# Optimization experiments

Measured on AMD Instinct MI355X. Metric: run time of the kernel, lower is better.

## Reference

```python
import jax, jax.numpy as jnp
import numpy as np

D_MODEL = 1024
D_STATE = 16
DT_RANK = 64  # d_model // 16 ('auto')
DT_MIN = 0.001
DT_MAX = 0.1


def setup_inputs() -> dict:
    key = jax.random.key(0)
    ks = jax.random.split(key, 7)
    B, S = 2, 2048
    return {
        "x": jax.random.normal(ks[0], (B, S, D_MODEL), jnp.float32),
        "w_in": jax.random.normal(ks[1], (D_MODEL, D_MODEL), jnp.float32) / np.sqrt(D_MODEL).astype(np.float32),
        "w_x": jax.random.normal(ks[2], (D_MODEL, DT_RANK + 2 * D_STATE), jnp.float32) / np.sqrt(D_MODEL).astype(np.float32),
        "w_dt": jax.random.normal(ks[3], (DT_RANK, D_MODEL), jnp.float32) / np.sqrt(DT_RANK).astype(np.float32),
        "b_dt": jnp.zeros((D_MODEL,), jnp.float32),
        "A_log": jax.random.normal(ks[5], (D_MODEL, D_STATE), jnp.float32) * 0.5,
        "Dp": jax.random.normal(ks[6], (D_MODEL,), jnp.float32),
    }


def reference(x, w_in, w_x, w_dt, b_dt, A_log, Dp):
    # x: (b, s, d)
    x_in = jnp.einsum('bsd,de->bse', x, w_in)          # in_proj, (b,s,d_inner=d)
    proj = jnp.einsum('bsd,dp->bsp', x_in, w_x)        # x_proj, (b,s,dt_rank+2n)
    dt_low, Bm, Cm = jnp.split(proj, [DT_RANK, DT_RANK + D_STATE], axis=-1)
    # dt_proj + softplus + range scaling -> (b,s,d)
    dt = jax.nn.softplus(jnp.einsum('bsr,rd->bsd', dt_low, w_dt) + b_dt) * (DT_MAX - DT_MIN) + DT_MIN
    A = -jnp.exp(A_log)                                # (d, n), strictly negative

    b, s, d = x.shape
    h0 = jnp.zeros((b, d, D_STATE), x.dtype)

    # time-major streams for scan
    dt_tm = jnp.swapaxes(dt, 0, 1)     # (s,b,d)
    u_tm = jnp.swapaxes(x_in, 0, 1)    # (s,b,d)
    B_tm = jnp.swapaxes(Bm, 0, 1)      # (s,b,n)
    C_tm = jnp.swapaxes(Cm, 0, 1)      # (s,b,n)

    def step(h, inp):
        dtt, ut, bt, ct = inp
        dA = dtt[:, :, None] * A                      # (b,d,n) = dt[b,d]*A[d,n]
        barA = jnp.exp(dA)
        # bar_B = dA; source sums the input term over channel dim d (keepdim)
        inp_term = jnp.einsum('bdn,bn,bd->bn', dA, bt, ut)  # (b,n)
        h = barA * h + inp_term[:, None, :]           # broadcast over d
        y = jnp.einsum('bdn,bn->bd', h, ct) + Dp * ut # (b,d)
        return h, y

    _, ys = jax.lax.scan(step, h0, (dt_tm, u_tm, B_tm, C_tm))  # ys: (s,b,d)
    return jnp.swapaxes(ys, 0, 1)                     # (b,s,d)
```

## Files before the change

kernel.cpp:

```cpp
#include <hip/hip_runtime.h>
#include <hip/hip_bf16.h>

#define D_MODEL 1024
#define D_STATE 16
#define DT_RANK 64
#define SEQ 2048
#define BATCH 2
#define M_TOTAL 4096
#define CHUNKS 64
#define CLEN 32

typedef __bf16 bf16x8 __attribute__((ext_vector_type(8)));
typedef float f32x4 __attribute__((ext_vector_type(4)));

__device__ __forceinline__ unsigned short f2bf(float f) {
    union { float f; unsigned int u; } v; v.f = f;
    unsigned int r = v.u + 0x7FFFu + ((v.u >> 16) & 1u);
    return (unsigned short)(r >> 16);
}
__device__ __forceinline__ float bf2f(unsigned short u) {
    union { unsigned int i; float f; } v; v.i = ((unsigned int)u) << 16; return v.f;
}
__device__ __forceinline__ void gload16(const void* g, void* l) {
    __builtin_amdgcn_global_load_lds(
        (const __attribute__((address_space(1))) unsigned int*)g,
        (__attribute__((address_space(3))) unsigned int*)l, 16, 0, 0);
}

__global__ void __launch_bounds__(256) k_setup(const float* __restrict__ x,
                                               const float* __restrict__ win,
                                               const float* __restrict__ wx,
                                               const float* __restrict__ alog,
                                               unsigned short* __restrict__ xb,
                                               unsigned short* __restrict__ wib,
                                               unsigned short* __restrict__ bt,
                                               unsigned short* __restrict__ wxT,
                                               unsigned short* __restrict__ wxBC,
                                               float* __restrict__ aneg,
                                               unsigned short* __restrict__ anegT) {
    __shared__ float tile[32][33];
    int blk = blockIdx.x;
    int t = threadIdx.x;
    if (blk < 4096) {
        int i = blk * 256 + t;
        float4 v = reinterpret_cast<const float4*>(x)[i];
        ushort4 o;
        o.x = f2bf(v.x); o.y = f2bf(v.y); o.z = f2bf(v.z); o.w = f2bf(v.w);
        reinterpret_cast<ushort4*>(xb)[i] = o;
    } else if (blk < 5120) {
        int i = (blk - 4096) * 256 + t;
        float4 v = reinterpret_cast<const float4*>(win)[i];
        ushort4 o;
        o.x = f2bf(v.x); o.y = f2bf(v.y); o.z = f2bf(v.z); o.w = f2bf(v.w);
        reinterpret_cast<ushort4*>(wib)[i] = o;
    } else if (blk < 6144) {
        int blk2 = blk - 5120;
        int bx = blk2 & 31, by = blk2 >> 5;
        int tx = t & 31, ty = t >> 5;
        int xc = bx * 32 + tx;
#pragma unroll
        for (int j = 0; j < 4; j++)
            tile[ty + 8 * j][tx] = win[(by * 32 + ty + 8 * j) * D_MODEL + xc];
        __syncthreads();
        int x2 = by * 32 + tx;
#pragma unroll
        for (int j = 0; j < 4; j++)
            bt[(bx * 32 + ty + 8 * j) * D_MODEL + x2] = f2bf(tile[tx][ty + 8 * j]);
    } else if (blk < 6400) {
        int idx = (blk - 6144) * 256 + t;
        int e = idx & 1023, p = idx >> 10;
        wxT[p * D_MODEL + e] = f2bf(wx[e * 96 + p]);
    } else if (blk < 6528) {
        int idx = (blk - 6400) * 256 + t;
        int e = idx & 1023, p = idx >> 10;
        wxBC[p * D_MODEL + e] = f2bf(wx[e * 96 + 64 + p]);
    } else {
        int i = (blk - 6528) * 256 + t;
        float v = -expf(alog[i]);
        aneg[i] = v;
        anegT[(i & 15) * D_MODEL + (i >> 4)] = f2bf(v);
    }
}

__global__ void __launch_bounds__(256) k_prepgemm(const unsigned short* __restrict__ wxT,
                                                  const unsigned short* __restrict__ wib,
                                                  float* __restrict__ Cp) {
    __shared__ unsigned short sA[2][64 * 32];
    __shared__ unsigned short sB[2][128 * 32];
    int bid = blockIdx.x;
    int n0 = (bid & 7) * 128;
    int ks = bid >> 3;
    int kbase = ks * 256;
    int t = threadIdx.x;
    int lane = t & 63;
    int w = t >> 6;
    int c = lane & 15, q = lane >> 4;

    const unsigned short* ga = wxT + (t >> 2) * D_MODEL + (t & 3) * 8 + kbase;
    const unsigned short* gb = wib + (n0 + (t >> 2)) * D_MODEL + (t & 3) * 8 + kbase;

    f32x4 acc[4][2] = {};
    {
        char* la = (char*)&sA[0][0] + w * 1024;
        char* lb = (char*)&sB[0][0] + w * 1024;
        gload16(ga, la);
        gload16(gb, lb);
        gload16(gb + 64 * D_MODEL, lb + 4096);
    }
    int cur = 0;
    for (int it = 0; it < 8; it++) {
        __syncthreads();
        if (it + 1 < 8) {
            int kn = (it + 1) * 32;
            char* la = (char*)&sA[cur ^ 1][0] + w * 1024;
            char* lb = (char*)&sB[cur ^ 1][0] + w * 1024;
            gload16(ga + kn, la);
            gload16(gb + kn, lb);
            gload16(gb + 64 * D_MODEL + kn, lb + 4096);
        }
        bf16x8 af[4], bfr[2];
#pragma unroll
        for (int i = 0; i < 4; i++)
            af[i] = *reinterpret_cast<const bf16x8*>(&sA[cur][(i * 16 + c) * 32 + q * 8]);
#pragma unroll
        for (int j = 0; j < 2; j++)
            bfr[j] = *reinterpret_cast<const bf16x8*>(&sB[cur][(w * 32 + j * 16 + c) * 32 + q * 8]);
#pragma unroll
        for (int i = 0; i < 4; i++)
#pragma unroll
            for (int j = 0; j < 2; j++)
                acc[i][j] = __builtin_amdgcn_mfma_f32_16x16x32_bf16(af[i], bfr[j], acc[i][j], 0, 0, 0);
        cur ^= 1;
    }
#pragma unroll
    for (int i = 0; i < 4; i++) {
        int p = i * 16 + q * 4;
#pragma unroll
        for (int j = 0; j < 2; j++) {
            int d = n0 + w * 32 + j * 16 + c;
#pragma unroll
            for (int r = 0; r < 4; r++)
                Cp[(ks * 64 + p + r) * D_MODEL + d] = acc[i][j][r];
        }
    }
}

__global__ void __launch_bounds__(256) k_prepreduce(const float* __restrict__ Cp,
                                                    float* __restrict__ Tt) {
    int idx = blockIdx.x * 256 + threadIdx.x;
    int d = idx & 1023;
    int p = idx >> 10;
    Tt[p * D_MODEL + d] = Cp[p * D_MODEL + d] + Cp[(64 + p) * D_MODEL + d] +
                          Cp[(128 + p) * D_MODEL + d] + Cp[(192 + p) * D_MODEL + d];
}

__global__ void __launch_bounds__(256) k_prep2(const float* __restrict__ wdt,
                                               const float* __restrict__ Tt,
                                               unsigned short* __restrict__ bt) {
    __shared__ float sw[DT_RANK][8];
    int m0 = blockIdx.x * 8;
    int tid = threadIdx.x;
    for (int s = tid; s < DT_RANK * 8; s += 256) {
        int r = s >> 3, rr = s & 7;
        sw[r][rr] = wdt[r * D_MODEL + m0 + rr];
    }
    __syncthreads();
    float acc[8][4] = {};
    for (int r = 0; r < DT_RANK; r++) {
        float tv0 = Tt[r * D_MODEL + tid];
        float tv1 = Tt[r * D_MODEL + tid + 256];
        float tv2 = Tt[r * D_MODEL + tid + 512];
        float tv3 = Tt[r * D_MODEL + tid + 768];
#pragma unroll
        for (int rr = 0; rr < 8; rr++) {
            float wv = sw[r][rr];
            acc[rr][0] = fmaf(wv, tv0, acc[rr][0]);
            acc[rr][1] = fmaf(wv, tv1, acc[rr][1]);
            acc[rr][2] = fmaf(wv, tv2, acc[rr][2]);
            acc[rr][3] = fmaf(wv, tv3, acc[rr][3]);
        }
    }
#pragma unroll
    for (int rr = 0; rr < 8; rr++)
#pragma unroll
        for (int i = 0; i < 4; i++)
            bt[(D_MODEL + m0 + rr) * D_MODEL + tid + i * 256] = f2bf(acc[rr][i]);
}

__global__ void __launch_bounds__(256) k_gemm_big(const unsigned short* __restrict__ xb,
                                                  const unsigned short* __restrict__ bt,
                                                  const float* __restrict__ bdt,
                                                  unsigned short* __restrict__ xinb,
                                                  unsigned short* __restrict__ dtb) {
    __shared__ unsigned short sA[2][128 * 64];
    __shared__ unsigned short sB[2][128 * 64];
    int bid = blockIdx.x;
    int m0 = (bid & 31) * 128;
    int nt = bid >> 5;
    int n0 = nt * 128;
    int t = threadIdx.x;
    int lane = t & 63;
    int w = t >> 6;
    int wm = (w >> 1) * 64, wn = (w & 1) * 64;
    int c = lane & 15, q = lane >> 4;

    const unsigned short* gA[4];
    const unsigned short* gB[4];
#pragma unroll
    for (int L = 0; L < 4; L++) {
        int s = L * 256 + t;
        int row = s >> 3, ch = (s & 7) ^ (row & 7);
        gA[L] = xb + (m0 + row) * D_MODEL + ch * 8;
        gB[L] = bt + (n0 + row) * D_MODEL + ch * 8;
    }

    f32x4 acc[4][4] = {};
    {
        char* la = (char*)&sA[0][0] + w * 1024;
        char* lb = (char*)&sB[0][0] + w * 1024;
#pragma unroll
        for (int L = 0; L < 4; L++) {
            gload16(gA[L], la + L * 4096);
            gload16(gB[L], lb + L * 4096);
        }
    }
    int cur = 0;
    for (int it = 0; it < 16; it++) {
        __syncthreads();
        if (it + 1 < 16) {
            int kn = (it + 1) * 64;
            char* la = (char*)&sA[cur ^ 1][0] + w * 1024;
            char* lb = (char*)&sB[cur ^ 1][0] + w * 1024;
#pragma unroll
            for (int L = 0; L < 4; L++) {
                gload16(gA[L] + kn, la + L * 4096);
                gload16(gB[L] + kn, lb + L * 4096);
            }
        }
#pragma unroll
        for (int kk = 0; kk < 2; kk++) {
            int perm = (((kk << 2) | q) ^ (c & 7)) << 3;
            bf16x8 af[4], bfr[4];
#pragma unroll
            for (int i = 0; i < 4; i++)
                af[i] = *reinterpret_cast<const bf16x8*>(&sA[cur][(wm + i * 16 + c) * 64 + perm]);
#pragma unroll
            for (int j = 0; j < 4; j++)
                bfr[j] = *reinterpret_cast<const bf16x8*>(&sB[cur][(wn + j * 16 + c) * 64 + perm]);
#pragma unroll
            for (int i = 0; i < 4; i++)
#pragma unroll
                for (int j = 0; j < 4; j++)
                    acc[i][j] = __builtin_amdgcn_mfma_f32_16x16x32_bf16(af[i], bfr[j], acc[i][j], 0, 0, 0);
        }
        cur ^= 1;
    }

    if (nt < 8) {
#pragma unroll
        for (int i = 0; i < 4; i++) {
            int row = m0 + wm + i * 16 + q * 4;
#pragma unroll
            for (int j = 0; j < 4; j++) {
                int col = n0 + wn + j * 16 + c;
#pragma unroll
                for (int r = 0; r < 4; r++)
                    xinb[(row + r) * D_MODEL + col] = f2bf(acc[i][j][r]);
            }
        }
    } else {
#pragma unroll
        for (int i = 0; i < 4; i++) {
            int row = m0 + wm + i * 16 + q * 4;
#pragma unroll
            for (int j = 0; j < 4; j++) {
                int dcol = n0 + wn + j * 16 + c - D_MODEL;
                float bv = bdt[dcol];
#pragma unroll
                for (int r = 0; r < 4; r++) {
                    float xv = acc[i][j][r] + bv;
                    float sp = fmaxf(xv, 0.f) + __logf(1.f + __expf(-fabsf(xv)));
                    dtb[(row + r) * D_MODEL + dcol] = f2bf(sp * 0.099f + 0.001f);
                }
            }
        }
    }
}

__global__ void __launch_bounds__(256) k_bcw(const unsigned short* __restrict__ xinb,
                                             const unsigned short* __restrict__ dtb,
                                             const unsigned short* __restrict__ wxBC,
                                             const unsigned short* __restrict__ anegT,
                                             float* __restrict__ bcp,
                                             float* __restrict__ wpp) {
    int bid = blockIdx.x;
    int m0 = (bid & 31) * 128;
    int ks = bid >> 5;
    int kbase = ks * 256;
    int t = threadIdx.x;
    int lane = t & 63, w = t >> 6;
    int c = lane & 15, q = lane >> 4;
    int mw = m0 + w * 32;
    f32x4 accb[2][2] = {};
    f32x4 accw[2] = {};
    const unsigned short* pa0 = xinb + (mw + c) * D_MODEL + kbase + q * 8;
    const unsigned short* pa1 = pa0 + 16 * D_MODEL;
    const unsigned short* pt0 = dtb + (mw + c) * D_MODEL + kbase + q * 8;
    const unsigned short* pt1 = pt0 + 16 * D_MODEL;
    const unsigned short* pb0 = wxBC + c * D_MODEL + kbase + q * 8;
    const unsigned short* pb1 = pb0 + 16 * D_MODEL;
    const unsigned short* pA = anegT + c * D_MODEL + kbase + q * 8;
#pragma unroll
    for (int k0 = 0; k0 < 256; k0 += 32) {
        bf16x8 a0 = *reinterpret_cast<const bf16x8*>(pa0 + k0);
        bf16x8 a1 = *reinterpret_cast<const bf16x8*>(pa1 + k0);
        bf16x8 t0 = *reinterpret_cast<const bf16x8*>(pt0 + k0);
        bf16x8 t1 = *reinterpret_cast<const bf16x8*>(pt1 + k0);
        bf16x8 b0 = *reinterpret_cast<const bf16x8*>(pb0 + k0);
        bf16x8 b1 = *reinterpret_cast<const bf16x8*>(pb1 + k0);
        bf16x8 bA = *reinterpret_cast<const bf16x8*>(pA + k0);
        bf16x8 g0, g1;
#pragma unroll
        for (int e = 0; e < 8; e++) {
            g0[e] = (__bf16)((float)t0[e] * (float)a0[e]);
            g1[e] = (__bf16)((float)t1[e] * (float)a1[e]);
        }
        accb[0][0] = __builtin_amdgcn_mfma_f32_16x16x32_bf16(a0, b0, accb[0][0], 0, 0, 0);
        accb[0][1] = __builtin_amdgcn_mfma_f32_16x16x32_bf16(a0, b1, accb[0][1], 0, 0, 0);
        accb[1][0] = __builtin_amdgcn_mfma_f32_16x16x32_bf16(a1, b0, accb[1][0], 0, 0, 0);
        accb[1][1] = __builtin_amdgcn_mfma_f32_16x16x32_bf16(a1, b1, accb[1][1], 0, 0, 0);
        accw[0] = __builtin_amdgcn_mfma_f32_16x16x32_bf16(g0, bA, accw[0], 0, 0, 0);
        accw[1] = __builtin_amdgcn_mfma_f32_16x16x32_bf16(g1, bA, accw[1], 0, 0, 0);
    }
#pragma unroll
    for (int i = 0; i < 2; i++) {
        int row = mw + i * 16 + q * 4;
#pragma unroll
        for (int j = 0; j < 2; j++) {
            int p = j * 16 + c;
#pragma unroll
            for (int r = 0; r < 4; r++)
                bcp[(ks * M_TOTAL + row + r) * 32 + p] = accb[i][j][r];
        }
#pragma unroll
        for (int r = 0; r < 4; r++)
            wpp[(ks * M_TOTAL + row + r) * 16 + c] = accw[i][r];
    }
}

__global__ void __launch_bounds__(256) k_fin(const float* __restrict__ bcp,
                                             const float* __restrict__ wpp,
                                             float* __restrict__ bc,
                                             float* __restrict__ winp) {
    int idx = blockIdx.x * 256 + threadIdx.x;
    int row = idx >> 5, p = idx & 31;
    float s = bcp[row * 32 + p] + bcp[(M_TOTAL + row) * 32 + p] +
              bcp[(2 * M_TOTAL + row) * 32 + p] + bcp[(3 * M_TOTAL + row) * 32 + p];
    bc[row * 32 + p] = s;
    if (p < 16) {
        float wsum = wpp[row * 16 + p] + wpp[(M_TOTAL + row) * 16 + p] +
                     wpp[(2 * M_TOTAL + row) * 16 + p] + wpp[(3 * M_TOTAL + row) * 16 + p];
        winp[row * 16 + p] = s * wsum;
    }
}

__global__ void __launch_bounds__(256) k_scan1(const unsigned short* __restrict__ dtb,
                                               const float* __restrict__ winp,
                                               const float* __restrict__ aneg,
                                               float* __restrict__ h_loc,
                                               float* __restrict__ dtsum) {
    __shared__ unsigned short s_dt[16][256];
    __shared__ float s_w[16][16];
    int dc = blockIdx.x & 3;
    int c = (blockIdx.x >> 2) & (CHUNKS - 1);
    int b = blockIdx.x >> 8;
    int tid = threadIdx.x;
    int d = dc * 256 + tid;
    float Ad[16];
    const float4* ar = reinterpret_cast<const float4*>(aneg + d * 16);
#pragma unroll
    for (int j = 0; j < 4; j++) {
        float4 a4 = ar[j];
        Ad[4 * j + 0] = a4.x; Ad[4 * j + 1] = a4.y;
        Ad[4 * j + 2] = a4.z; Ad[4 * j + 3] = a4.w;
    }
    float h[16];
#pragma unroll
    for (int n = 0; n < 16; n++) h[n] = 0.f;
    float dts = 0.f;

    int r8 = tid >> 5, col8 = (tid & 31) * 8;
    for (int t0 = 0; t0 < CLEN; t0 += 16) {
        __syncthreads();
        int rowbase = b * SEQ + c * CLEN + t0;
        *reinterpret_cast<uint4*>(&s_dt[r8][col8]) =
            *reinterpret_cast<const uint4*>(dtb + (rowbase + r8) * D_MODEL + dc * 256 + col8);
        *reinterpret_cast<uint4*>(&s_dt[8 + r8][col8]) =
            *reinterpret_cast<const uint4*>(dtb + (rowbase + 8 + r8) * D_MODEL + dc * 256 + col8);
        {
            int r = tid >> 4, n = tid & 15;
            s_w[r][n] = winp[(rowbase + r) * 16 + n];
        }
        __syncthreads();
        for (int r = 0; r < 16; r++) {
            float dtv = bf2f(s_dt[r][tid]);
            dts += dtv;
#pragma unroll
            for (int n = 0; n < 16; n++) {
                float ba = __expf(dtv * Ad[n]);
                h[n] = fmaf(ba, h[n], s_w[r][n]);
            }
        }
    }
    int base = ((b * CHUNKS + c) * D_MODEL + d) * 16;
#pragma unroll
    for (int j = 0; j < 4; j++) {
        f32x4 v = {h[4 * j], h[4 * j + 1], h[4 * j + 2], h[4 * j + 3]};
        *reinterpret_cast<f32x4*>(h_loc + base + 4 * j) = v;
    }
    dtsum[(b * CHUNKS + c) * D_MODEL + d] = dts;
}

__global__ void __launch_bounds__(256) k_scan2(float* __restrict__ h_inout,
                                               const float* __restrict__ dtsum,
                                               const float* __restrict__ aneg) {
    int idx = blockIdx.x * 256 + threadIdx.x;
    int n = idx & 15;
    int d = (idx >> 4) & (D_MODEL - 1);
    int b = idx >> 14;
    float A = aneg[d * 16 + n];
    float H = 0.f;
    int off = (b * CHUNKS) * D_MODEL + d;
    float hl = h_inout[off * 16 + n];
    float ds = dtsum[off];
    for (int c = 0; c < CHUNKS; c++) {
        int off2 = off + D_MODEL;
        float hl_n = 0.f, ds_n = 0.f;
        if (c + 1 < CHUNKS) { hl_n = h_inout[off2 * 16 + n]; ds_n = dtsum[off2]; }
        float P = __expf(ds * A);
        h_inout[off * 16 + n] = H;
        H = fmaf(P, H, hl);
        hl = hl_n; ds = ds_n; off = off2;
    }
}

__global__ void __launch_bounds__(256) k_scan3(const unsigned short* __restrict__ dtb,
                                               const unsigned short* __restrict__ xinb,
                                               const float* __restrict__ winp,
                                               const float* __restrict__ bc,
                                               const float* __restrict__ aneg,
                                               const float* __restrict__ dp,
                                               const float* __restrict__ H_in,
                                               float* __restrict__ out) {
    __shared__ unsigned short s_dt[16][256], s_u[16][256];
    __shared__ float s_w[16][16], s_c[16][16];
    int dc = blockIdx.x & 3;
    int c = (blockIdx.x >> 2) & (CHUNKS - 1);
    int b = blockIdx.x >> 8;
    int tid = threadIdx.x;
    int d = dc * 256 + tid;
    float Ad[16];
    const float4* ar = reinterpret_cast<const float4*>(aneg + d * 16);
#pragma unroll
    for (int j = 0; j < 4; j++) {
        float4 a4 = ar[j];
        Ad[4 * j + 0] = a4.x; Ad[4 * j + 1] = a4.y;
        Ad[4 * j + 2] = a4.z; Ad[4 * j + 3] = a4.w;
    }
    float Dpd = dp[d];
    float h[16];
    int base = ((b * CHUNKS + c) * D_MODEL + d) * 16;
#pragma unroll
    for (int j = 0; j < 4; j++) {
        f32x4 v = *reinterpret_cast<const f32x4*>(H_in + base + 4 * j);
        h[4 * j] = v[0]; h[4 * j + 1] = v[1]; h[4 * j + 2] = v[2]; h[4 * j + 3] = v[3];
    }

    int r8 = tid >> 5, col8 = (tid & 31) * 8;
    for (int t0 = 0; t0 < CLEN; t0 += 16) {
        __syncthreads();
        int rowbase = b * SEQ + c * CLEN + t0;
        *reinterpret_cast<uint4*>(&s_dt[r8][col8]) =
            *reinterpret_cast<const uint4*>(dtb + (rowbase + r8) * D_MODEL + dc * 256 + col8);
        *reinterpret_cast<uint4*>(&s_dt[8 + r8][col8]) =
            *reinterpret_cast<const uint4*>(dtb + (rowbase + 8 + r8) * D_MODEL + dc * 256 + col8);
        *reinterpret_cast<uint4*>(&s_u[r8][col8]) =
            *reinterpret_cast<const uint4*>(xinb + (rowbase + r8) * D_MODEL + dc * 256 + col8);
        *reinterpret_cast<uint4*>(&s_u[8 + r8][col8]) =
            *reinterpret_cast<const uint4*>(xinb + (rowbase + 8 + r8) * D_MODEL + dc * 256 + col8);
        {
            int r = tid >> 4, n = tid & 15;
            s_w[r][n] = winp[(rowbase + r) * 16 + n];
            s_c[r][n] = bc[(rowbase + r) * 32 + 16 + n];
        }
        __syncthreads();
        for (int r = 0; r < 16; r++) {
            float dtv = bf2f(s_dt[r][tid]), uv = bf2f(s_u[r][tid]);
            float y = Dpd * uv;
#pragma unroll
            for (int n = 0; n < 16; n++) {
                float ba = __expf(dtv * Ad[n]);
                h[n] = fmaf(ba, h[n], s_w[r][n]);
                y = fmaf(h[n], s_c[r][n], y);
            }
            out[(rowbase + r) * D_MODEL + d] = y;
        }
    }
}

extern "C" void kernel_launch(void* const* d_in, const int* in_sizes, int n_in,
                              void* d_out, int out_size, void* d_ws, size_t ws_size,
                              hipStream_t stream) {
    const float* x     = (const float*)d_in[0];
    const float* w_in  = (const float*)d_in[1];
    const float* w_x   = (const float*)d_in[2];
    const float* w_dt  = (const float*)d_in[3];
    const float* b_dt  = (const float*)d_in[4];
    const float* A_log = (const float*)d_in[5];
    const float* Dp    = (const float*)d_in[6];
    float* out = (float*)d_out;

    char* ws = (char*)d_ws;
    unsigned short* xb   = (unsigned short*)(ws + 0);
    unsigned short* bt   = (unsigned short*)(ws + 8388608);
    float* Tt            = (float*)(ws + 12845056);
    float* aneg          = (float*)(ws + 13107200);
    float* bc            = (float*)(ws + 13172736);
    float* winp          = (float*)(ws + 13697024);
    unsigned short* xinb = (unsigned short*)(ws + 13959168);
    unsigned short* dtb  = (unsigned short*)(ws + 22347776);
    unsigned short* wib  = (unsigned short*)(ws + 22347776);
    unsigned short* wxT  = (unsigned short*)(ws + 24444928);
    float* Cp            = (float*)(ws + 24707072);
    unsigned short* wxBC = (unsigned short*)(ws + 30736384);
    float* bcp           = (float*)(ws + 30801920);
    float* wpp           = (float*)(ws + 32899072);
    unsigned short* anegT= (unsigned short*)(ws + 33947648);
    float* h_loc         = (float*)(ws + 0);
    float* dtsum         = (float*)(ws + 8388608);

    k_setup<<<6592, 256, 0, stream>>>(x, w_in, w_x, A_log, xb, wib, bt, wxT, wxBC, aneg, anegT);
    k_prepgemm<<<32, 256, 0, stream>>>(wxT, wib, Cp);
    k_prepreduce<<<256, 256, 0, stream>>>(Cp, Tt);
    k_prep2<<<128, 256, 0, stream>>>(w_dt, Tt, bt);
    k_gemm_big<<<512, 256, 0, stream>>>(xb, bt, b_dt, xinb, dtb);
    k_bcw<<<128, 256, 0, stream>>>(xinb, dtb, wxBC, anegT, bcp, wpp);
    k_fin<<<512, 256, 0, stream>>>(bcp, wpp, bc, winp);
    k_scan1<<<BATCH * CHUNKS * 4, 256, 0, stream>>>(dtb, winp, aneg, h_loc, dtsum);
    k_scan2<<<128, 256, 0, stream>>>(h_loc, dtsum, aneg);
    k_scan3<<<BATCH * CHUNKS * 4, 256, 0, stream>>>(dtb, xinb, winp, bc, aneg, Dp, h_loc, out);
}
```

Baseline: 176.5 us.

## Fuse split-K reduction into scans, vectorize GEMM stores, use exp2 in scans

Removes the k_fin kernel so the scan kernels sum the split-K partials for B, C and the input weight themselves. Doubles the split-K factor in the prep and bcw GEMMs for more parallelism. Swaps the MFMA operands so each lane holds four contiguous output columns and can issue vector stores. Pre-scales A by log2(e) so the scans can call the native exp2, and batches the loads in the k_scan2 chunk loop. In exchange the scans repeat the partial-sum reads per block, and the workspace layout is moved to fit the larger partial buffers.

```diff
diff --git a/kernel.cpp b/kernel.cpp
--- a/kernel.cpp
+++ b/kernel.cpp
@@ -9,6 +9,7 @@
 #define M_TOTAL 4096
 #define CHUNKS 64
 #define CLEN 32
+#define LOG2E 1.44269504088896f
 
 typedef __bf16 bf16x8 __attribute__((ext_vector_type(8)));
 typedef float f32x4 __attribute__((ext_vector_type(4)));
@@ -26,6 +27,7 @@
         (const __attribute__((address_space(1))) unsigned int*)g,
         (__attribute__((address_space(3))) unsigned int*)l, 16, 0, 0);
 }
+__device__ __forceinline__ float fexp2(float x) { return __builtin_amdgcn_exp2f(x); }
 
 __global__ void __launch_bounds__(256) k_setup(const float* __restrict__ x,
                                                const float* __restrict__ win,
@@ -77,7 +79,7 @@
     } else {
         int i = (blk - 6528) * 256 + t;
         float v = -expf(alog[i]);
-        aneg[i] = v;
+        aneg[i] = v * LOG2E;
         anegT[(i & 15) * D_MODEL + (i >> 4)] = f2bf(v);
     }
 }
@@ -90,7 +92,7 @@
     int bid = blockIdx.x;
     int n0 = (bid & 7) * 128;
     int ks = bid >> 3;
-    int kbase = ks * 256;
+    int kbase = ks * 128;
     int t = threadIdx.x;
     int lane = t & 63;
     int w = t >> 6;
@@ -108,9 +110,9 @@
         gload16(gb + 64 * D_MODEL, lb + 4096);
     }
     int cur = 0;
-    for (int it = 0; it < 8; it++) {
-        __syncthreads();
-        if (it + 1 < 8) {
+    for (int it = 0; it < 4; it++) {
+        __syncthreads();
+        if (it + 1 < 4) {
             int kn = (it + 1) * 32;
             char* la = (char*)&sA[cur ^ 1][0] + w * 1024;
             char* lb = (char*)&sB[cur ^ 1][0] + w * 1024;
@@ -129,18 +131,16 @@
         for (int i = 0; i < 4; i++)
 #pragma unroll
             for (int j = 0; j < 2; j++)
-                acc[i][j] = __builtin_amdgcn_mfma_f32_16x16x32_bf16(af[i], bfr[j], acc[i][j], 0, 0, 0);
+                acc[i][j] = __builtin_amdgcn_mfma_f32_16x16x32_bf16(bfr[j], af[i], acc[i][j], 0, 0, 0);
         cur ^= 1;
     }
 #pragma unroll
     for (int i = 0; i < 4; i++) {
-        int p = i * 16 + q * 4;
+        int p = ks * 64 + i * 16 + c;
 #pragma unroll
         for (int j = 0; j < 2; j++) {
-            int d = n0 + w * 32 + j * 16 + c;
-#pragma unroll
-            for (int r = 0; r < 4; r++)
-                Cp[(ks * 64 + p + r) * D_MODEL + d] = acc[i][j][r];
+            int d = n0 + w * 32 + j * 16 + q * 4;
+            *reinterpret_cast<f32x4*>(&Cp[p * D_MODEL + d]) = acc[i][j];
         }
     }
 }
@@ -148,10 +148,10 @@
 __global__ void __launch_bounds__(256) k_prepreduce(const float* __restrict__ Cp,
                                                     float* __restrict__ Tt) {
     int idx = blockIdx.x * 256 + threadIdx.x;
-    int d = idx & 1023;
-    int p = idx >> 10;
-    Tt[p * D_MODEL + d] = Cp[p * D_MODEL + d] + Cp[(64 + p) * D_MODEL + d] +
-                          Cp[(128 + p) * D_MODEL + d] + Cp[(192 + p) * D_MODEL + d];
+    float s = 0.f;
+#pragma unroll
+    for (int ks = 0; ks < 8; ks++) s += Cp[ks * 65536 + idx];
+    Tt[idx] = s;
 }
 
 __global__ void __launch_bounds__(256) k_prep2(const float* __restrict__ wdt,
@@ -251,7 +251,7 @@
             for (int i = 0; i < 4; i++)
 #pragma unroll
                 for (int j = 0; j < 4; j++)
-                    acc[i][j] = __builtin_amdgcn_mfma_f32_16x16x32_bf16(af[i], bfr[j], acc[i][j], 0, 0, 0);
+                    acc[i][j] = __builtin_amdgcn_mfma_f32_16x16x32_bf16(bfr[j], af[i], acc[i][j], 0, 0, 0);
         }
         cur ^= 1;
     }
@@ -259,29 +259,46 @@
     if (nt < 8) {
 #pragma unroll
         for (int i = 0; i < 4; i++) {
-            int row = m0 + wm + i * 16 + q * 4;
+            int row = m0 + wm + i * 16 + c;
 #pragma unroll
             for (int j = 0; j < 4; j++) {
-                int col = n0 + wn + j * 16 + c;
-#pragma unroll
-                for (int r = 0; r < 4; r++)
-                    xinb[(row + r) * D_MODEL + col] = f2bf(acc[i][j][r]);
+                int col = n0 + wn + j * 16 + q * 4;
+                ushort4 o;
+                o.x = f2bf(acc[i][j][0]); o.y = f2bf(acc[i][j][1]);
+                o.z = f2bf(acc[i][j][2]); o.w = f2bf(acc[i][j][3]);
+                *reinterpret_cast<ushort4*>(&xinb[row * D_MODEL + col]) = o;
             }
         }
     } else {
 #pragma unroll
         for (int i = 0; i < 4; i++) {
-            int row = m0 + wm + i * 16 + q * 4;
+            int row = m0 + wm + i * 16 + c;
 #pragma unroll
             for (int j = 0; j < 4; j++) {
-                int dcol = n0 + wn + j * 16 + c - D_MODEL;
-                float bv = bdt[dcol];
-#pragma unroll
-                for (int r = 0; r < 4; r++) {
-                    float xv = acc[i][j][r] + bv;
+                int dcol = n0 + wn + j * 16 + q * 4 - D_MODEL;
+                float4 bv = *reinterpret_cast<const float4*>(&bdt[dcol]);
+                ushort4 o;
+                {
+                    float xv = acc[i][j][0] + bv.x;
                     float sp = fmaxf(xv, 0.f) + __logf(1.f + __expf(-fabsf(xv)));
-                    dtb[(row + r) * D_MODEL + dcol] = f2bf(sp * 0.099f + 0.001f);
+                    o.x = f2bf(sp * 0.099f + 0.001f);
                 }
+                {
+                    float xv = acc[i][j][1] + bv.y;
+                    float sp = fmaxf(xv, 0.f) + __logf(1.f + __expf(-fabsf(xv)));
+                    o.y = f2bf(sp * 0.099f + 0.001f);
+                }
+                {
+                    float xv = acc[i][j][2] + bv.z;
+                    float sp = fmaxf(xv, 0.f) + __logf(1.f + __expf(-fabsf(xv)));
+                    o.z = f2bf(sp * 0.099f + 0.001f);
+                }
+                {
+                    float xv = acc[i][j][3] + bv.w;
+                    float sp = fmaxf(xv, 0.f) + __logf(1.f + __expf(-fabsf(xv)));
+                    o.w = f2bf(sp * 0.099f + 0.001f);
+                }
+                *reinterpret_cast<ushort4*>(&dtb[row * D_MODEL + dcol]) = o;
             }
         }
     }
@@ -296,7 +313,7 @@
     int bid = blockIdx.x;
     int m0 = (bid & 31) * 128;
     int ks = bid >> 5;
-    int kbase = ks * 256;
+    int kbase = ks * 128;
     int t = threadIdx.x;
     int lane = t & 63, w = t >> 6;
     int c = lane & 15, q = lane >> 4;
@@ -311,7 +328,7 @@
     const unsigned short* pb1 = pb0 + 16 * D_MODEL;
     const unsigned short* pA = anegT + c * D_MODEL + kbase + q * 8;
 #pragma unroll
-    for (int k0 = 0; k0 < 256; k0 += 32) {
+    for (int k0 = 0; k0 < 128; k0 += 32) {
         bf16x8 a0 = *reinterpret_cast<const bf16x8*>(pa0 + k0);
         bf16x8 a1 = *reinterpret_cast<const bf16x8*>(pa1 + k0);
         bf16x8 t0 = *reinterpret_cast<const bf16x8*>(pt0 + k0);
@@ -325,47 +342,26 @@
             g0[e] = (__bf16)((float)t0[e] * (float)a0[e]);
             g1[e] = (__bf16)((float)t1[e] * (float)a1[e]);
         }
-        accb[0][0] = __builtin_amdgcn_mfma_f32_16x16x32_bf16(a0, b0, accb[0][0], 0, 0, 0);
-        accb[0][1] = __builtin_amdgcn_mfma_f32_16x16x32_bf16(a0, b1, accb[0][1], 0, 0, 0);
-        accb[1][0] = __builtin_amdgcn_mfma_f32_16x16x32_bf16(a1, b0, accb[1][0], 0, 0, 0);
-        accb[1][1] = __builtin_amdgcn_mfma_f32_16x16x32_bf16(a1, b1, accb[1][1], 0, 0, 0);
-        accw[0] = __builtin_amdgcn_mfma_f32_16x16x32_bf16(g0, bA, accw[0], 0, 0, 0);
-        accw[1] = __builtin_amdgcn_mfma_f32_16x16x32_bf16(g1, bA, accw[1], 0, 0, 0);
+        accb[0][0] = __builtin_amdgcn_mfma_f32_16x16x32_bf16(b0, a0, accb[0][0], 0, 0, 0);
+        accb[0][1] = __builtin_amdgcn_mfma_f32_16x16x32_bf16(b1, a0, accb[0][1], 0, 0, 0);
+        accb[1][0] = __builtin_amdgcn_mfma_f32_16x16x32_bf16(b0, a1, accb[1][0], 0, 0, 0);
+        accb[1][1] = __builtin_amdgcn_mfma_f32_16x16x32_bf16(b1, a1, accb[1][1], 0, 0, 0);
+        accw[0] = __builtin_amdgcn_mfma_f32_16x16x32_bf16(bA, g0, accw[0], 0, 0, 0);
+        accw[1] = __builtin_amdgcn_mfma_f32_16x16x32_bf16(bA, g1, accw[1], 0, 0, 0);
     }
 #pragma unroll
     for (int i = 0; i < 2; i++) {
-        int row = mw + i * 16 + q * 4;
-#pragma unroll
-        for (int j = 0; j < 2; j++) {
-            int p = j * 16 + c;
-#pragma unroll
-            for (int r = 0; r < 4; r++)
-                bcp[(ks * M_TOTAL + row + r) * 32 + p] = accb[i][j][r];
-        }
-#pragma unroll
-        for (int r = 0; r < 4; r++)
-            wpp[(ks * M_TOTAL + row + r) * 16 + c] = accw[i][r];
-    }
-}
-
-__global__ void __launch_bounds__(256) k_fin(const float* __restrict__ bcp,
-                                             const float* __restrict__ wpp,
-                                             float* __restrict__ bc,
-                                             float* __restrict__ winp) {
-    int idx = blockIdx.x * 256 + threadIdx.x;
-    int row = idx >> 5, p = idx & 31;
-    float s = bcp[row * 32 + p] + bcp[(M_TOTAL + row) * 32 + p] +
-              bcp[(2 * M_TOTAL + row) * 32 + p] + bcp[(3 * M_TOTAL + row) * 32 + p];
-    bc[row * 32 + p] = s;
-    if (p < 16) {
-        float wsum = wpp[row * 16 + p] + wpp[(M_TOTAL + row) * 16 + p] +
-                     wpp[(2 * M_TOTAL + row) * 16 + p] + wpp[(3 * M_TOTAL + row) * 16 + p];
-        winp[row * 16 + p] = s * wsum;
+        int row = mw + i * 16 + c;
+#pragma unroll
+        for (int j = 0; j < 2; j++)
+            *reinterpret_cast<f32x4*>(&bcp[(ks * M_TOTAL + row) * 32 + j * 16 + q * 4]) = accb[i][j];
+        *reinterpret_cast<f32x4*>(&wpp[(ks * M_TOTAL + row) * 16 + q * 4]) = accw[i];
     }
 }
 
 __global__ void __launch_bounds__(256) k_scan1(const unsigned short* __restrict__ dtb,
-                                               const float* __restrict__ winp,
+                                               const float* __restrict__ bcp,
+                                               const float* __restrict__ wpp,
                                                const float* __restrict__ aneg,
                                                float* __restrict__ h_loc,
                                                float* __restrict__ dtsum) {
@@ -399,7 +395,14 @@
             *reinterpret_cast<const uint4*>(dtb + (rowbase + 8 + r8) * D_MODEL + dc * 256 + col8);
         {
             int r = tid >> 4, n = tid & 15;
-            s_w[r][n] = winp[(rowbase + r) * 16 + n];
+            int row = rowbase + r;
+            float sB = 0.f, sw = 0.f;
+#pragma unroll
+            for (int ks = 0; ks < 8; ks++) {
+                sB += bcp[(ks * M_TOTAL + row) * 32 + n];
+                sw += wpp[(ks * M_TOTAL + row) * 16 + n];
+            }
+            s_w[r][n] = sB * sw;
         }
         __syncthreads();
         for (int r = 0; r < 16; r++) {
@@ -407,7 +410,7 @@
             dts += dtv;
 #pragma unroll
             for (int n = 0; n < 16; n++) {
-                float ba = __expf(dtv * Ad[n]);
+                float ba = fexp2(dtv * Ad[n]);
                 h[n] = fmaf(ba, h[n], s_w[r][n]);
             }
         }
@@ -421,33 +424,39 @@
     dtsum[(b * CHUNKS + c) * D_MODEL + d] = dts;
 }
 
-__global__ void __launch_bounds__(256) k_scan2(float* __restrict__ h_inout,
+__global__ void __launch_bounds__(128) k_scan2(float* __restrict__ h_inout,
                                                const float* __restrict__ dtsum,
                                                const float* __restrict__ aneg) {
-    int idx = blockIdx.x * 256 + threadIdx.x;
+    int idx = blockIdx.x * 128 + threadIdx.x;
     int n = idx & 15;
     int d = (idx >> 4) & (D_MODEL - 1);
     int b = idx >> 14;
     float A = aneg[d * 16 + n];
     float H = 0.f;
-    int off = (b * CHUNKS) * D_MODEL + d;
-    float hl = h_inout[off * 16 + n];
-    float ds = dtsum[off];
-    for (int c = 0; c < CHUNKS; c++) {
-        int off2 = off + D_MODEL;
-        float hl_n = 0.f, ds_n = 0.f;
-        if (c + 1 < CHUNKS) { hl_n = h_inout[off2 * 16 + n]; ds_n = dtsum[off2]; }
-        float P = __expf(ds * A);
-        h_inout[off * 16 + n] = H;
-        H = fmaf(P, H, hl);
-        hl = hl_n; ds = ds_n; off = off2;
+    int off0 = b * CHUNKS * D_MODEL + d;
+#pragma unroll 1
+    for (int g = 0; g < CHUNKS; g += 8) {
+        float hl[8], ds[8];
+#pragma unroll
+        for (int j = 0; j < 8; j++) {
+            int off = off0 + (g + j) * D_MODEL;
+            hl[j] = h_inout[off * 16 + n];
+            ds[j] = dtsum[off];
+        }
+#pragma unroll
+        for (int j = 0; j < 8; j++) {
+            int off = off0 + (g + j) * D_MODEL;
+            float P = fexp2(ds[j] * A);
+            h_inout[off * 16 + n] = H;
+            H = fmaf(P, H, hl[j]);
+        }
     }
 }
 
 __global__ void __launch_bounds__(256) k_scan3(const unsigned short* __restrict__ dtb,
                                                const unsigned short* __restrict__ xinb,
-                                               const float* __restrict__ winp,
-                                               const float* __restrict__ bc,
+                                               const float* __restrict__ bcp,
+                                               const float* __restrict__ wpp,
                                                const float* __restrict__ aneg,
                                                const float* __restrict__ dp,
                                                const float* __restrict__ H_in,
@@ -490,8 +499,16 @@
             *reinterpret_cast<const uint4*>(xinb + (rowbase + 8 + r8) * D_MODEL + dc * 256 + col8);
         {
             int r = tid >> 4, n = tid & 15;
-            s_w[r][n] = winp[(rowbase + r) * 16 + n];
-            s_c[r][n] = bc[(rowbase + r) * 32 + 16 + n];
+            int row = rowbase + r;
+            float sB = 0.f, sw = 0.f, sC = 0.f;
+#pragma unroll
+            for (int ks = 0; ks < 8; ks++) {
+                sB += bcp[(ks * M_TOTAL + row) * 32 + n];
+                sC += bcp[(ks * M_TOTAL + row) * 32 + 16 + n];
+                sw += wpp[(ks * M_TOTAL + row) * 16 + n];
+            }
+            s_w[r][n] = sB * sw;
+            s_c[r][n] = sC;
         }
         __syncthreads();
         for (int r = 0; r < 16; r++) {
@@ -499,7 +516,7 @@
             float y = Dpd * uv;
 #pragma unroll
             for (int n = 0; n < 16; n++) {
-                float ba = __expf(dtv * Ad[n]);
+                float ba = fexp2(dtv * Ad[n]);
                 h[n] = fmaf(ba, h[n], s_w[r][n]);
                 y = fmaf(h[n], s_c[r][n], y);
             }
@@ -525,8 +542,6 @@
     unsigned short* bt   = (unsigned short*)(ws + 8388608);
     float* Tt            = (float*)(ws + 12845056);
     float* aneg          = (float*)(ws + 13107200);
-    float* bc            = (float*)(ws + 13172736);
-    float* winp          = (float*)(ws + 13697024);
     unsigned short* xinb = (unsigned short*)(ws + 13959168);
     unsigned short* dtb  = (unsigned short*)(ws + 22347776);
     unsigned short* wib  = (unsigned short*)(ws + 22347776);
@@ -534,19 +549,18 @@
     float* Cp            = (float*)(ws + 24707072);
     unsigned short* wxBC = (unsigned short*)(ws + 30736384);
     float* bcp           = (float*)(ws + 30801920);
-    float* wpp           = (float*)(ws + 32899072);
-    unsigned short* anegT= (unsigned short*)(ws + 33947648);
+    float* wpp           = (float*)(ws + 34996224);
+    unsigned short* anegT= (unsigned short*)(ws + 37093376);
     float* h_loc         = (float*)(ws + 0);
     float* dtsum         = (float*)(ws + 8388608);
 
     k_setup<<<6592, 256, 0, stream>>>(x, w_in, w_x, A_log, xb, wib, bt, wxT, wxBC, aneg, anegT);
-    k_prepgemm<<<32, 256, 0, stream>>>(wxT, wib, Cp);
+    k_prepgemm<<<64, 256, 0, stream>>>(wxT, wib, Cp);
     k_prepreduce<<<256, 256, 0, stream>>>(Cp, Tt);
     k_prep2<<<128, 256, 0, stream>>>(w_dt, Tt, bt);
     k_gemm_big<<<512, 256, 0, stream>>>(xb, bt, b_dt, xinb, dtb);
-    k_bcw<<<128, 256, 0, stream>>>(xinb, dtb, wxBC, anegT, bcp, wpp);
-    k_fin<<<512, 256, 0, stream>>>(bcp, wpp, bc, winp);
-    k_scan1<<<BATCH * CHUNKS * 4, 256, 0, stream>>>(dtb, winp, aneg, h_loc, dtsum);
-    k_scan2<<<128, 256, 0, stream>>>(h_loc, dtsum, aneg);
-    k_scan3<<<BATCH * CHUNKS * 4, 256, 0, stream>>>(dtb, xinb, winp, bc, aneg, Dp, h_loc, out);
-}
+    k_bcw<<<256, 256, 0, stream>>>(xinb, dtb, wxBC, anegT, bcp, wpp);
+    k_scan1<<<BATCH * CHUNKS * 4, 256, 0, stream>>>(dtb, bcp, wpp, aneg, h_loc, dtsum);
+    k_scan2<<<256, 128, 0, stream>>>(h_loc, dtsum, aneg);
+    k_scan3<<<BATCH * CHUNKS * 4, 256, 0, stream>>>(dtb, xinb, bcp, wpp, aneg, Dp, h_loc, out);
+}
```

Result: no change. 175.7 us (-0.4%).
